# Kernel tuning notes

Hardware: AMD Instinct MI355X
Metric: run time of the kernel (lower is better)

The kernel has to match this reference:

```python
import jax, jax.numpy as jnp
import numpy as np

N, E, IN, ED, C, L, S, R, G, OUT = 100000, 400000, 64, 16, 128, 3, 2, 4, 4096, 128

def _glorot(k, shape):
    return jax.random.normal(k, shape, dtype=jnp.float32) / jnp.sqrt(jnp.float32(shape[-1]))

def setup_inputs():
    key = jax.random.key(0)
    ks = jax.random.split(key, 16)
    return {
        "x": jax.random.normal(ks[0], (N, IN), jnp.float32),
        "edge_attr": jax.random.normal(ks[1], (E, ED), jnp.float32),
        "lin_a_w": _glorot(ks[2], (C, IN)),
        "lin_a_b": jnp.zeros((C,), jnp.float32),
        "lin_b_w": _glorot(ks[3], (C, ED)),
        "lin_b_b": jnp.zeros((C,), jnp.float32),
        "wn": _glorot(ks[4], (L, C, C)),
        "we": _glorot(ks[5], (L, C, C)),
        "bil_w": _glorot(ks[6], (L, S, C, C)),
        "lin_w": _glorot(ks[7], (L, S, 3 * C)),
        "lin_bias": jnp.zeros((L, S), jnp.float32),
        "gate_w": _glorot(ks[8], (L, C, 3 * C)),
        "gate_b": jnp.zeros((L, C), jnp.float32),
        "att_w1": _glorot(ks[9], (L, C // R, C)),
        "att_w2": _glorot(ks[10], (L, C, C // R)),
        "out_w": _glorot(ks[11], (OUT, C)),
        "out_b": jnp.zeros((OUT,), jnp.float32),
        "edge_index": jax.random.randint(ks[12], (2, E), 0, N),
        "batch": jnp.sort(jax.random.randint(ks[13], (N,), 0, G)),
        "xgb_flag": 0,
    }

def reference(x, edge_attr, lin_a_w, lin_a_b, lin_b_w, lin_b_b, wn, we, bil_w,
              lin_w, lin_bias, gate_w, gate_b, att_w1, att_w2, out_w, out_b,
              edge_index, batch, xgb_flag):
    src, dst = edge_index[0], edge_index[1]  # PyG: row 0 = source j, row 1 = target i
    h = jax.nn.relu(x @ lin_a_w.T + lin_a_b)          # [N, C]
    e = jax.nn.relu(edge_attr @ lin_b_w.T + lin_b_b)  # [E, C]
    for l in range(L):
        # ---- NTNConv ----
        xn = h @ wn[l]                                 # node transform
        en = e @ we[l]                                 # edge transform
        x_i, x_j = xn[dst], xn[src]                    # [E, C] gathers
        score = jnp.einsum('ec,scd,ed->es', x_i, bil_w[l], x_j)          # bilinear attn [E, S]
        block = jnp.concatenate([x_i, en, x_j], axis=1) @ lin_w[l].T + lin_bias[l]
        alpha = jnp.tanh(score + block)                # [E, S]; dropout is identity in eval
        msg = jnp.maximum(x_j, en).reshape(E, S, C // S) * alpha[:, :, None]
        hh = jax.nn.relu(jax.ops.segment_sum(msg.reshape(E, C), dst, num_segments=N))
        # ---- gated residual ----
        beta = jax.nn.sigmoid(jnp.concatenate([h, hh, h - hh], axis=1) @ gate_w[l].T + gate_b[l])
        h = beta * h + (1.0 - beta) * hh
        # ---- FeatureAttention (scatter max/sum SE block) ----
        mx = jax.ops.segment_max(h, batch, num_segments=G)
        mx = jnp.where(jnp.isneginf(mx), 0.0, mx)      # empty segments -> 0 (torch_scatter zero-init)
        sm = jax.ops.segment_sum(h, batch, num_segments=G)
        mlp = lambda z: jax.nn.relu(z @ att_w1[l].T) @ att_w2[l].T
        y = jax.nn.sigmoid(mlp(mx) + mlp(sm))          # [G, C]
        h = h * y[batch]
    mol = jax.nn.relu(jax.ops.segment_sum(h, batch, num_segments=G))  # global_add_pool
    return mol @ out_w.T + out_b                       # [G, OUT]
```

## Files before the change

kernel.cpp:

```cpp
#include <hip/hip_runtime.h>
#include <cstdint>
#include <cstddef>

#define N_NODES 100000
#define N_EDGES 400000
#define IN_F 64
#define ED_F 16
#define C_F 128
#define L_LAYERS 3
#define G_GRAPHS 4096
#define OUT_F 128

#define BM 128
#define BN 128
#define BK 32
#define TM 8

template<bool WT, bool RELUA, int ACT, bool BIAS, bool A2S>
__global__ __launch_bounds__(256) void gemm_kernel(
    const float* __restrict__ A, const float* __restrict__ A2,
    const float* __restrict__ W, const float* __restrict__ bias,
    float* __restrict__ out, int M, int K, int Nn, int wld)
{
  __shared__ float As[BK][BM + 4];
  __shared__ float Ws[BK][BN];
  const int tid = threadIdx.x;
  const int tx = tid & 15;
  const int ty = tid >> 4;
  const int m0 = blockIdx.y * BM;
  const int n0 = blockIdx.x * BN;
  float acc[TM][8];
#pragma unroll
  for (int i = 0; i < TM; i++)
#pragma unroll
    for (int j = 0; j < 8; j++) acc[i][j] = 0.f;

  for (int k0 = 0; k0 < K; k0 += BK) {
#pragma unroll
    for (int i = 0; i < 16; i++) {
      int idx = tid + i * 256;
      int k = idx & 31, m = idx >> 5;
      int gm = m0 + m, gk = k0 + k;
      float v = 0.f;
      if (gm < M && gk < K) {
        if (A2S) {
          v = (gk < C_F) ? A[(size_t)gm * C_F + gk]
                         : fmaxf(A2[(size_t)gm * C_F + (gk - C_F)], 0.f);
        } else {
          v = A[(size_t)gm * K + gk];
          if (RELUA) v = fmaxf(v, 0.f);
        }
      }
      As[k][m] = v;
    }
#pragma unroll
    for (int i = 0; i < 16; i++) {
      int idx = tid + i * 256;
      int n = idx & 127, k = idx >> 7;
      int gn = n0 + n, gk = k0 + k;
      float v = 0.f;
      if (gn < Nn && gk < K)
        v = WT ? W[(size_t)gn * K + gk] : W[(size_t)gk * wld + gn];
      Ws[k][n] = v;
    }
    __syncthreads();
#pragma unroll
    for (int kk = 0; kk < BK; kk++) {
      float a[TM], b[8];
#pragma unroll
      for (int i = 0; i < TM; i++) a[i] = As[kk][ty * TM + i];
#pragma unroll
      for (int j = 0; j < 4; j++) {
        b[j]     = Ws[kk][tx * 4 + j];
        b[4 + j] = Ws[kk][64 + tx * 4 + j];
      }
#pragma unroll
      for (int i = 0; i < TM; i++)
#pragma unroll
        for (int j = 0; j < 8; j++) acc[i][j] += a[i] * b[j];
    }
    __syncthreads();
  }
#pragma unroll
  for (int i = 0; i < TM; i++) {
    int gm = m0 + ty * TM + i;
    if (gm >= M) continue;
#pragma unroll
    for (int j = 0; j < 8; j++) {
      int gn = n0 + ((j < 4) ? (tx * 4 + j) : (64 + tx * 4 + (j - 4)));
      if (gn >= Nn) continue;
      float v = acc[i][j];
      if (BIAS) v += bias[gn];
      if (ACT == 1) v = fmaxf(v, 0.f);
      else if (ACT == 2) v = 1.f / (1.f + expf(-v));
      out[(size_t)gm * Nn + gn] = v;
    }
  }
}

__global__ void zero_kernel(float* __restrict__ p, int n)
{
  int i = blockIdx.x * 256 + threadIdx.x;
  if (i < n) p[i] = 0.f;
}

__global__ void pack_kernel(const float* __restrict__ bil_w,
                            const float* __restrict__ gate_w,
                            float* __restrict__ bil2, float* __restrict__ gw, int l)
{
  int i = blockIdx.x * 256 + threadIdx.x;
  if (i < 32768) {
    int c = i >> 8, sd = i & 255, s = sd >> 7, d = sd & 127;
    bil2[i] = bil_w[(((size_t)l * 2 + s) * 128 + c) * 128 + d];
  } else if (i < 65536) {
    int j = i - 32768;
    int k = j >> 7, n = j & 127;
    const float* g = gate_w + (size_t)l * 128 * 384 + (size_t)n * 384;
    gw[j] = (k < 128) ? (g[k] + g[256 + k]) : (g[k] - g[k + 128]);
  }
}

__global__ __launch_bounds__(256) void p_kernel(const float* __restrict__ xn,
    const float* __restrict__ lin_w_l, float* __restrict__ p, int Nn)
{
  int node = (blockIdx.x * 256 + threadIdx.x) >> 6;
  int lane = threadIdx.x & 63;
  if (node >= Nn) return;
  const float* r = xn + (size_t)node * C_F;
  float v0 = r[lane], v1 = r[lane + 64];
  float pi0 = v0 * lin_w_l[lane]       + v1 * lin_w_l[64 + lane];
  float pi1 = v0 * lin_w_l[384 + lane] + v1 * lin_w_l[448 + lane];
  float pj0 = v0 * lin_w_l[256 + lane] + v1 * lin_w_l[320 + lane];
  float pj1 = v0 * lin_w_l[640 + lane] + v1 * lin_w_l[704 + lane];
#pragma unroll
  for (int off = 32; off > 0; off >>= 1) {
    pi0 += __shfl_xor(pi0, off); pi1 += __shfl_xor(pi1, off);
    pj0 += __shfl_xor(pj0, off); pj1 += __shfl_xor(pj1, off);
  }
  if (lane == 0) {
    p[(size_t)node * 4 + 0] = pi0; p[(size_t)node * 4 + 1] = pi1;
    p[(size_t)node * 4 + 2] = pj0; p[(size_t)node * 4 + 3] = pj1;
  }
}

#define EPB 64
__global__ __launch_bounds__(256) void edge_fused(
    const float* __restrict__ xn, const float* __restrict__ z,
    const float* __restrict__ edge_attr, const float* __restrict__ p,
    const float* __restrict__ lbw, const float* __restrict__ lbb,
    const float* __restrict__ weL, const float* __restrict__ lin_w_l,
    const float* __restrict__ lin_bias_l, const int* __restrict__ ei,
    float* __restrict__ hh)
{
  __shared__ float e_s[4][4][128];
  const int tid = threadIdx.x;
  const int wave = tid >> 6, lane = tid & 63;
  const int c0 = lane * 2;

  const float4* r0 = (const float4*)(lbw + (size_t)c0 * ED_F);
  const float4* r1 = (const float4*)(lbw + (size_t)(c0 + 1) * ED_F);
  float4 w0a = r0[0], w0b = r0[1], w0c = r0[2], w0d = r0[3];
  float4 w1a = r1[0], w1b = r1[1], w1c = r1[2], w1d = r1[3];
  float bb0 = lbb[c0], bb1 = lbb[c0 + 1];
  float lw0a = lin_w_l[128 + c0], lw0b = lin_w_l[129 + c0];
  float lw1a = lin_w_l[512 + c0], lw1b = lin_w_l[513 + c0];
  float lbias0 = lin_bias_l[0], lbias1 = lin_bias_l[1];

  const int ebase = blockIdx.x * EPB + wave * 16;

  for (int g = 0; g < 4; g++) {
    const int e0 = ebase + g * 4;
#pragma unroll
    for (int j = 0; j < 4; j++) {
      const float4* ar = (const float4*)(edge_attr + (size_t)(e0 + j) * ED_F);
      float4 a0 = ar[0], a1 = ar[1], a2 = ar[2], a3 = ar[3];
      float acc0 = bb0, acc1 = bb1;
      acc0 += a0.x*w0a.x + a0.y*w0a.y + a0.z*w0a.z + a0.w*w0a.w;
      acc0 += a1.x*w0b.x + a1.y*w0b.y + a1.z*w0b.z + a1.w*w0b.w;
      acc0 += a2.x*w0c.x + a2.y*w0c.y + a2.z*w0c.z + a2.w*w0c.w;
      acc0 += a3.x*w0d.x + a3.y*w0d.y + a3.z*w0d.z + a3.w*w0d.w;
      acc1 += a0.x*w1a.x + a0.y*w1a.y + a0.z*w1a.z + a0.w*w1a.w;
      acc1 += a1.x*w1b.x + a1.y*w1b.y + a1.z*w1b.z + a1.w*w1b.w;
      acc1 += a2.x*w1c.x + a2.y*w1c.y + a2.z*w1c.z + a2.w*w1c.w;
      acc1 += a3.x*w1d.x + a3.y*w1d.y + a3.z*w1d.z + a3.w*w1d.w;
      float2 ev = make_float2(fmaxf(acc0, 0.f), fmaxf(acc1, 0.f));
      ((float2*)e_s[wave][j])[lane] = ev;
    }
    __builtin_amdgcn_wave_barrier();

    float ena[4] = {0.f, 0.f, 0.f, 0.f}, enb[4] = {0.f, 0.f, 0.f, 0.f};
#pragma unroll 8
    for (int k = 0; k < 128; k++) {
      float2 wv = *(const float2*)(weL + (size_t)k * C_F + c0);
#pragma unroll
      for (int j = 0; j < 4; j++) {
        float ev = e_s[wave][j][k];
        ena[j] += ev * wv.x;
        enb[j] += ev * wv.y;
      }
    }
    __builtin_amdgcn_wave_barrier();

#pragma unroll
    for (int j = 0; j < 4; j++) {
      int e = e0 + j;
      int sidx = ei[e];
      int didx = ei[N_EDGES + e];
      float2 xj = *(const float2*)(xn + (size_t)sidx * C_F + c0);
      float2 z0 = *(const float2*)(z + (size_t)didx * 256 + c0);
      float2 z1 = *(const float2*)(z + (size_t)didx * 256 + 128 + c0);
      float rr0 = z0.x * xj.x + z0.y * xj.y + ena[j] * lw0a + enb[j] * lw0b;
      float rr1 = z1.x * xj.x + z1.y * xj.y + ena[j] * lw1a + enb[j] * lw1b;
#pragma unroll
      for (int off = 32; off > 0; off >>= 1) {
        rr0 += __shfl_xor(rr0, off);
        rr1 += __shfl_xor(rr1, off);
      }
      float al0 = tanhf(rr0 + p[(size_t)didx * 4 + 0] + p[(size_t)sidx * 4 + 2] + lbias0);
      float al1 = tanhf(rr1 + p[(size_t)didx * 4 + 1] + p[(size_t)sidx * 4 + 3] + lbias1);
      float aj = (lane < 32) ? al0 : al1;
      atomicAdd(&hh[(size_t)didx * C_F + c0],     fmaxf(xj.x, ena[j]) * aj);
      atomicAdd(&hh[(size_t)didx * C_F + c0 + 1], fmaxf(xj.y, enb[j]) * aj);
    }
  }
}

__global__ void update_kernel(float* __restrict__ h, const float* __restrict__ hh,
                              const float* __restrict__ beta, int total)
{
  int i = blockIdx.x * 256 + threadIdx.x;
  if (i >= total) return;
  float b = beta[i];
  h[i] = b * h[i] + (1.f - b) * fmaxf(hh[i], 0.f);
}

template<bool DOMAX>
__global__ __launch_bounds__(256) void seg_kernel(const float* __restrict__ h,
    const int* __restrict__ batch, float* __restrict__ sm, float* __restrict__ mx, int Nn)
{
  int c = threadIdx.x & 127;
  int half = threadIdx.x >> 7;
  int nbase = blockIdx.x * 16 + half * 8;
  float asum = 0.f, amax = 0.f; int cur = -1;
  for (int i = 0; i < 8; i++) {
    int n = nbase + i;
    if (n >= Nn) break;
    int g = batch[n];
    float v = h[(size_t)n * C_F + c];
    if (g != cur) {
      if (cur >= 0) {
        atomicAdd(&sm[(size_t)cur * C_F + c], asum);
        if (DOMAX) atomicMax((int*)&mx[(size_t)cur * C_F + c], __float_as_int(amax));
      }
      cur = g; asum = 0.f; amax = 0.f;
    }
    asum += v;
    if (DOMAX) amax = fmaxf(amax, v);
  }
  if (cur >= 0) {
    atomicAdd(&sm[(size_t)cur * C_F + c], asum);
    if (DOMAX) atomicMax((int*)&mx[(size_t)cur * C_F + c], __float_as_int(amax));
  }
}

__global__ __launch_bounds__(128) void featmlp(const float* __restrict__ mx,
    const float* __restrict__ sm, const float* __restrict__ w1,
    const float* __restrict__ w2, float* __restrict__ y)
{
  __shared__ float smx[128], ssm[128], t1[32], t2[32];
  int g = blockIdx.x; int t = threadIdx.x;
  smx[t] = mx[(size_t)g * 128 + t];
  ssm[t] = sm[(size_t)g * 128 + t];
  __syncthreads();
  if (t < 32) {
    float a1 = 0.f, a2 = 0.f;
    for (int c = 0; c < 128; c++) {
      float w = w1[t * 128 + c];
      a1 += smx[c] * w; a2 += ssm[c] * w;
    }
    t1[t] = fmaxf(a1, 0.f); t2[t] = fmaxf(a2, 0.f);
  }
  __syncthreads();
  float a = 0.f;
  for (int j = 0; j < 32; j++) a += (t1[j] + t2[j]) * w2[t * 32 + j];
  y[(size_t)g * 128 + t] = 1.f / (1.f + expf(-a));
}

__global__ void scale_kernel(float* __restrict__ h, const float* __restrict__ y,
                             const int* __restrict__ batch, int total)
{
  int i = blockIdx.x * 256 + threadIdx.x;
  if (i >= total) return;
  h[i] *= y[(size_t)batch[i >> 7] * C_F + (i & 127)];
}

extern "C" void kernel_launch(void* const* d_in, const int* in_sizes, int n_in,
                              void* d_out, int out_size, void* d_ws, size_t ws_size,
                              hipStream_t stream)
{
  const float* x         = (const float*)d_in[0];
  const float* edge_attr = (const float*)d_in[1];
  const float* lin_a_w   = (const float*)d_in[2];
  const float* lin_a_b   = (const float*)d_in[3];
  const float* lin_b_w   = (const float*)d_in[4];
  const float* lin_b_b   = (const float*)d_in[5];
  const float* wn        = (const float*)d_in[6];
  const float* we        = (const float*)d_in[7];
  const float* bil_w     = (const float*)d_in[8];
  const float* lin_w     = (const float*)d_in[9];
  const float* lin_bias  = (const float*)d_in[10];
  const float* gate_w    = (const float*)d_in[11];
  const float* gate_b    = (const float*)d_in[12];
  const float* att_w1    = (const float*)d_in[13];
  const float* att_w2    = (const float*)d_in[14];
  const float* out_w     = (const float*)d_in[15];
  const float* out_b     = (const float*)d_in[16];
  const int*   ei        = (const int*)d_in[17];
  const int*   batch     = (const int*)d_in[18];
  (void)in_sizes; (void)n_in;

  float* ws = (float*)d_ws;
  const size_t availf = ws_size / sizeof(float);
  const size_t NH = (size_t)N_NODES * C_F;
  const size_t GH = (size_t)G_GRAPHS * C_F;

  size_t off = 0;
  float* h    = ws + off; off += NH;
  float* xn   = ws + off; off += NH;
  float* hh   = ws + off; off += NH;
  float* p    = ws + off; off += (size_t)N_NODES * 4;
  float* mx   = ws + off; off += GH;
  float* smv  = ws + off; off += GH;
  float* yv   = ws + off; off += GH;
  float* mol  = ws + off; off += GH;
  float* bil2 = ws + off; off += 32768;
  float* gw   = ws + off; off += 32768;
  float* z    = ws + off; off += (size_t)N_NODES * 256;
  float* beta = z;

  dim3 blk(256);
  if (off > availf) {
    zero_kernel<<<dim3((out_size + 255) / 256), blk, 0, stream>>>((float*)d_out, out_size);
    return;
  }

  const int total_h = N_NODES * C_F;

  gemm_kernel<true, false, 1, true, false><<<dim3(1, (N_NODES + BM - 1) / BM), blk, 0, stream>>>(
      x, nullptr, lin_a_w, lin_a_b, h, N_NODES, IN_F, C_F, C_F);

  for (int l = 0; l < L_LAYERS; l++) {
    pack_kernel<<<dim3(256), blk, 0, stream>>>(bil_w, gate_w, bil2, gw, l);
    gemm_kernel<false, false, 0, false, false><<<dim3(1, (N_NODES + BM - 1) / BM), blk, 0, stream>>>(
        h, nullptr, wn + (size_t)l * C_F * C_F, nullptr, xn, N_NODES, C_F, C_F, C_F);
    gemm_kernel<false, false, 0, false, false><<<dim3(2, (N_NODES + BM - 1) / BM), blk, 0, stream>>>(
        xn, nullptr, bil2, nullptr, z, N_NODES, C_F, 256, 256);
    p_kernel<<<dim3((N_NODES * 64 + 255) / 256), blk, 0, stream>>>(
        xn, lin_w + (size_t)l * 768, p, N_NODES);

    zero_kernel<<<dim3((total_h + 255) / 256), blk, 0, stream>>>(hh, total_h);
    edge_fused<<<dim3(N_EDGES / EPB), blk, 0, stream>>>(
        xn, z, edge_attr, p, lin_b_w, lin_b_b, we + (size_t)l * C_F * C_F,
        lin_w + (size_t)l * 768, lin_bias + (size_t)l * 2, ei, hh);

    gemm_kernel<false, false, 2, true, true><<<dim3(1, (N_NODES + BM - 1) / BM), blk, 0, stream>>>(
        h, hh, gw, gate_b + (size_t)l * C_F, beta, N_NODES, 256, C_F, C_F);
    update_kernel<<<dim3((total_h + 255) / 256), blk, 0, stream>>>(h, hh, beta, total_h);

    zero_kernel<<<dim3((int)(2 * GH + 255) / 256), blk, 0, stream>>>(mx, (int)(2 * GH));
    seg_kernel<true><<<dim3((N_NODES + 15) / 16), blk, 0, stream>>>(h, batch, smv, mx, N_NODES);
    featmlp<<<dim3(G_GRAPHS), dim3(128), 0, stream>>>(
        mx, smv, att_w1 + (size_t)l * 32 * 128, att_w2 + (size_t)l * 128 * 32, yv);
    scale_kernel<<<dim3((total_h + 255) / 256), blk, 0, stream>>>(h, yv, batch, total_h);
  }

  zero_kernel<<<dim3((int)(GH + 255) / 256), blk, 0, stream>>>(mol, (int)GH);
  seg_kernel<false><<<dim3((N_NODES + 15) / 16), blk, 0, stream>>>(h, batch, mol, nullptr, N_NODES);
  gemm_kernel<true, true, 0, true, false><<<dim3(1, (G_GRAPHS + BM - 1) / BM), blk, 0, stream>>>(
      mol, nullptr, out_w, out_b, (float*)d_out, G_GRAPHS, C_F, OUT_F, OUT_F);
}
```

Measured before the change: 5.607 ms.

## Precompute wn·bil2 and fuse node transform and bilinear GEMMs

Precomputes the product of the layer's node weight and the packed bilinear weight into a 128x384 combined matrix, using a small GEMM on the weights. A single GEMM from h then produces both xn and z, with split output writes. This removes the serial dependency on xn and one full pass that reads xn, at the cost of an extra tiny weight GEMM and pack work. It also changes floating-point association order.

```diff
diff --git a/kernel.cpp b/kernel.cpp
--- a/kernel.cpp
+++ b/kernel.cpp
@@ -16,11 +16,12 @@
 #define BK 32
 #define TM 8
 
-template<bool WT, bool RELUA, int ACT, bool BIAS, bool A2S>
+template<bool WT, bool RELUA, int ACT, bool BIAS, bool A2S, int OMODE>
 __global__ __launch_bounds__(256) void gemm_kernel(
     const float* __restrict__ A, const float* __restrict__ A2,
     const float* __restrict__ W, const float* __restrict__ bias,
-    float* __restrict__ out, int M, int K, int Nn, int wld)
+    float* __restrict__ out, float* __restrict__ out2,
+    int M, int K, int Nn, int wld, int old)
 {
   __shared__ float As[BK][BM + 4];
   __shared__ float Ws[BK][BN];
@@ -93,7 +94,12 @@
       if (BIAS) v += bias[gn];
       if (ACT == 1) v = fmaxf(v, 0.f);
       else if (ACT == 2) v = 1.f / (1.f + expf(-v));
-      out[(size_t)gm * Nn + gn] = v;
+      if (OMODE == 0) {
+        out[(size_t)gm * old + gn] = v;
+      } else {
+        if (gn < C_F) out[(size_t)gm * C_F + gn] = v;
+        else          out2[(size_t)gm * 256 + (gn - C_F)] = v;
+      }
     }
   }
 }
@@ -106,7 +112,9 @@
 
 __global__ void pack_kernel(const float* __restrict__ bil_w,
                             const float* __restrict__ gate_w,
-                            float* __restrict__ bil2, float* __restrict__ gw, int l)
+                            const float* __restrict__ wn,
+                            float* __restrict__ bil2, float* __restrict__ gw,
+                            float* __restrict__ Wz, int l)
 {
   int i = blockIdx.x * 256 + threadIdx.x;
   if (i < 32768) {
@@ -117,6 +125,10 @@
     int k = j >> 7, n = j & 127;
     const float* g = gate_w + (size_t)l * 128 * 384 + (size_t)n * 384;
     gw[j] = (k < 128) ? (g[k] + g[256 + k]) : (g[k] - g[k + 128]);
+  } else if (i < 81920) {
+    int j = i - 65536;
+    int k = j >> 7, n = j & 127;
+    Wz[(size_t)k * 384 + n] = wn[(size_t)l * 16384 + j];
   }
 }
 
@@ -335,6 +347,7 @@
   float* mol  = ws + off; off += GH;
   float* bil2 = ws + off; off += 32768;
   float* gw   = ws + off; off += 32768;
+  float* Wz   = ws + off; off += 49152;
   float* z    = ws + off; off += (size_t)N_NODES * 256;
   float* beta = z;
 
@@ -346,15 +359,15 @@
 
   const int total_h = N_NODES * C_F;
 
-  gemm_kernel<true, false, 1, true, false><<<dim3(1, (N_NODES + BM - 1) / BM), blk, 0, stream>>>(
-      x, nullptr, lin_a_w, lin_a_b, h, N_NODES, IN_F, C_F, C_F);
+  gemm_kernel<true, false, 1, true, false, 0><<<dim3(1, (N_NODES + BM - 1) / BM), blk, 0, stream>>>(
+      x, nullptr, lin_a_w, lin_a_b, h, nullptr, N_NODES, IN_F, C_F, C_F, C_F);
 
   for (int l = 0; l < L_LAYERS; l++) {
-    pack_kernel<<<dim3(256), blk, 0, stream>>>(bil_w, gate_w, bil2, gw, l);
-    gemm_kernel<false, false, 0, false, false><<<dim3(1, (N_NODES + BM - 1) / BM), blk, 0, stream>>>(
-        h, nullptr, wn + (size_t)l * C_F * C_F, nullptr, xn, N_NODES, C_F, C_F, C_F);
-    gemm_kernel<false, false, 0, false, false><<<dim3(2, (N_NODES + BM - 1) / BM), blk, 0, stream>>>(
-        xn, nullptr, bil2, nullptr, z, N_NODES, C_F, 256, 256);
+    pack_kernel<<<dim3(320), blk, 0, stream>>>(bil_w, gate_w, wn, bil2, gw, Wz, l);
+    gemm_kernel<false, false, 0, false, false, 0><<<dim3(2, 1), blk, 0, stream>>>(
+        wn + (size_t)l * 16384, nullptr, bil2, nullptr, Wz + 128, nullptr, 128, C_F, 256, 256, 384);
+    gemm_kernel<false, false, 0, false, false, 1><<<dim3(3, (N_NODES + BM - 1) / BM), blk, 0, stream>>>(
+        h, nullptr, Wz, nullptr, xn, z, N_NODES, C_F, 384, 384, 0);
     p_kernel<<<dim3((N_NODES * 64 + 255) / 256), blk, 0, stream>>>(
         xn, lin_w + (size_t)l * 768, p, N_NODES);
 
@@ -363,8 +376,8 @@
         xn, z, edge_attr, p, lin_b_w, lin_b_b, we + (size_t)l * C_F * C_F,
         lin_w + (size_t)l * 768, lin_bias + (size_t)l * 2, ei, hh);
 
-    gemm_kernel<false, false, 2, true, true><<<dim3(1, (N_NODES + BM - 1) / BM), blk, 0, stream>>>(
-        h, hh, gw, gate_b + (size_t)l * C_F, beta, N_NODES, 256, C_F, C_F);
+    gemm_kernel<false, false, 2, true, true, 0><<<dim3(1, (N_NODES + BM - 1) / BM), blk, 0, stream>>>(
+        h, hh, gw, gate_b + (size_t)l * C_F, beta, nullptr, N_NODES, 256, C_F, C_F, C_F);
     update_kernel<<<dim3((total_h + 255) / 256), blk, 0, stream>>>(h, hh, beta, total_h);
 
     zero_kernel<<<dim3((int)(2 * GH + 255) / 256), blk, 0, stream>>>(mx, (int)(2 * GH));
@@ -376,6 +389,6 @@
 
   zero_kernel<<<dim3((int)(GH + 255) / 256), blk, 0, stream>>>(mol, (int)GH);
   seg_kernel<false><<<dim3((N_NODES + 15) / 16), blk, 0, stream>>>(h, batch, mol, nullptr, N_NODES);
-  gemm_kernel<true, true, 0, true, false><<<dim3(1, (G_GRAPHS + BM - 1) / BM), blk, 0, stream>>>(
-      mol, nullptr, out_w, out_b, (float*)d_out, G_GRAPHS, C_F, OUT_F, OUT_F);
-}
+  gemm_kernel<true, true, 0, true, false, 0><<<dim3(1, (G_GRAPHS + BM - 1) / BM), blk, 0, stream>>>(
+      mol, nullptr, out_w, out_b, (float*)d_out, nullptr, G_GRAPHS, C_F, OUT_F, OUT_F, OUT_F);
+}
```

Result: no change. 5.562 ms (-0.8%).
